# Kernel optimization log

Hardware: AMD Instinct MI355X
Metric: run time of the kernel (lower is better)

Reference implementation:

```python
import jax, jax.numpy as jnp
import numpy as np

B, S, H = 2, 2048, 2048
NH, NKV, HD = 16, 4, 128
THETA = 1000000.0

def _rope_tables(seq_len, dim, theta):
    inv_freq = 1.0 / (theta ** (np.arange(0, dim, 2, dtype=np.float32) / dim))
    t = np.arange(seq_len, dtype=np.float32)
    freqs = np.outer(t, inv_freq)                      # [S, dim/2]
    emb = np.concatenate([freqs, freqs], axis=-1)      # [S, dim]
    return jnp.asarray(np.cos(emb)), jnp.asarray(np.sin(emb))

def setup_inputs() -> dict:
    key = jax.random.key(0)
    ks = jax.random.split(key, 5)
    cos, sin = _rope_tables(S, HD, THETA)
    scale = 1.0 / np.sqrt(H)
    return {
        "x": jax.random.normal(ks[0], (B, S, H), jnp.float32),
        "cos": cos, "sin": sin,
        "wq": jax.random.normal(ks[1], (H, NH * HD), jnp.float32) * scale,
        "wk": jax.random.normal(ks[2], (H, NKV * HD), jnp.float32) * scale,
        "wv": jax.random.normal(ks[3], (H, NKV * HD), jnp.float32) * scale,
        "wo": jax.random.normal(ks[4], (NH * HD, H), jnp.float32) * scale,
    }

def _rotate_half(t):
    h = t.shape[-1] // 2
    return jnp.concatenate([-t[..., h:], t[..., :h]], axis=-1)

def reference(x, cos, sin, wq, wk, wv, wo):
    b, s, _ = x.shape
    n_rep = NH // NKV
    q = (x @ wq).reshape(b, s, NH, HD)    # [b,s,nh,hd]
    k = (x @ wk).reshape(b, s, NKV, HD)
    v = (x @ wv).reshape(b, s, NKV, HD)
    # RoPE: cos/sin [s,hd] broadcast over batch and heads
    c = cos[None, :, None, :]
    sn = sin[None, :, None, :]
    q = q * c + _rotate_half(q) * sn
    k = k * c + _rotate_half(k) * sn
    # GQA: repeat kv heads n_rep times
    k = jnp.repeat(k, n_rep, axis=2)      # [b,s,nh,hd]
    v = jnp.repeat(v, n_rep, axis=2)
    q = q.transpose(0, 2, 1, 3)           # [b,nh,s,hd]
    k = k.transpose(0, 2, 1, 3)
    v = v.transpose(0, 2, 1, 3)
    scores = jnp.einsum('bhqd,bhkd->bhqk', q, k) / jnp.sqrt(jnp.float32(HD))
    causal = jnp.tril(jnp.ones((s, s), dtype=bool))
    scores = jnp.where(causal[None, None], scores, jnp.float32(-jnp.inf))
    attn = jax.nn.softmax(scores.astype(jnp.float32), axis=-1).astype(q.dtype)
    out = jnp.einsum('bhqk,bhkd->bhqd', attn, v)
    out = out.transpose(0, 2, 1, 3).reshape(b, s, NH * HD)
    return out @ wo
```

## Files before the change

kernel.cpp:

```cpp
#include <hip/hip_runtime.h>
#include <hip/hip_bf16.h>

#define Bb 2
#define Ss 2048
#define Hh 2048
#define NH 16
#define NKV 4
#define HD 128
#define NREP (NH / NKV)
#define Mrows (Bb * Ss)
#define NQKV (NH*HD + 2*NKV*HD)

using short8 = __attribute__((ext_vector_type(8))) short;
using f32x4  = __attribute__((ext_vector_type(4))) float;

__device__ __forceinline__ unsigned short f2b(float f) {
  union { float f; unsigned u; } v; v.f = f;
  return (unsigned short)((v.u + 0x7fffu + ((v.u >> 16) & 1u)) >> 16);
}

__device__ __forceinline__ void gload16(const void* g, void* l) {
  __builtin_amdgcn_global_load_lds(
      (const __attribute__((address_space(1))) unsigned int*)g,
      (__attribute__((address_space(3))) unsigned int*)l, 16, 0, 0);
}

__global__ void prep(const float* __restrict__ x, unsigned short* __restrict__ xb,
                     const float* __restrict__ wq, const float* __restrict__ wk,
                     const float* __restrict__ wv, unsigned short* __restrict__ wqkvt,
                     const float* __restrict__ wo, unsigned short* __restrict__ wot) {
  __shared__ float tile[32][33];
  const int bid = blockIdx.x;
  const int t = threadIdx.x;
  if (bid < 8192) {
    int i = (bid * 256 + t) * 4;
    float4 f = *(const float4*)(x + i);
    ushort4 o;
    o.x = f2b(f.x); o.y = f2b(f.y); o.z = f2b(f.z); o.w = f2b(f.w);
    *(ushort4*)(xb + i) = o;
    return;
  }
  const int tx = t & 31, ty = t >> 5;
  if (bid < 8192 + 6144) {
    int idx = bid - 8192;
    int n0 = (idx % 96) * 32, k0 = (idx / 96) * 32;
    const float* src; int base, C;
    if (n0 < Hh)            { src = wq; base = 0;        C = NH * HD; }
    else if (n0 < Hh + 512) { src = wk; base = Hh;       C = NKV * HD; }
    else                    { src = wv; base = Hh + 512; C = NKV * HD; }
    int ng = n0 + tx;
    int cmg = ng;
    if (ng < Hh + 512) {
      int j = ng & 127;
      cmg = (ng & ~127) + ((j >> 5) << 4) + (j & 15) + ((j >> 4) & 1) * 64;
    }
    int col = cmg - base;
    #pragma unroll
    for (int i = ty; i < 32; i += 8)
      tile[i][tx] = src[(long)(k0 + i) * C + col];
    __syncthreads();
    #pragma unroll
    for (int i = ty; i < 32; i += 8)
      wqkvt[(long)(n0 + i) * Hh + k0 + tx] = f2b(tile[tx][i]);
  } else {
    int idx = bid - 8192 - 6144;
    int n0 = (idx % 64) * 32, k0 = (idx / 64) * 32;
    #pragma unroll
    for (int i = ty; i < 32; i += 8)
      tile[i][tx] = wo[(long)(k0 + i) * Hh + n0 + tx];
    __syncthreads();
    #pragma unroll
    for (int i = ty; i < 32; i += 8)
      wot[(long)(n0 + i) * Hh + k0 + tx] = f2b(tile[tx][i]);
  }
}

__global__ __launch_bounds__(512, 2) void gemm_qkv(const unsigned short* __restrict__ A,
                                                   const unsigned short* __restrict__ Bt,
                                                   const float* __restrict__ cosT,
                                                   const float* __restrict__ sinT,
                                                   unsigned short* __restrict__ qt,
                                                   unsigned short* __restrict__ kt,
                                                   unsigned short* __restrict__ vt) {
  __shared__ unsigned short As[2][256 * 64];
  __shared__ unsigned short Bs[2][256 * 64];
  const int t = threadIdx.x;
  const int lane = t & 63, wid = t >> 6;
  const int quad = lane >> 4, l16 = lane & 15;
  const int nt = blockIdx.x >> 4, mt = blockIdx.x & 15;
  const int n0 = nt * 256, m0 = mt * 256;
  const int wm = (wid >> 2) * 128, wn = (wid & 3) * 64;
  const bool isv = nt >= 10;
  const int Kk = Hh;

  const int sg = (lane & 7) ^ (lane >> 3);
  const int srow = wid * 8 + (lane >> 3);
  const unsigned short* Ag = A  + (long)(m0 + srow) * Kk + sg * 8;
  const unsigned short* Bg = Bt + (long)(n0 + srow) * Kk + sg * 8;

  f32x4 acc[8][4] = {};
  short8 aH[4][2], bH[2][2];

#define STAGE_A(buf, k0) { _Pragma("unroll") for (int i = 0; i < 4; i++) \
    gload16(Ag + (long)i * 64 * Kk + (k0), &As[buf][wid * 512 + i * 4096]); }
#define STAGE_B(buf, k0) { _Pragma("unroll") for (int i = 0; i < 4; i++) \
    gload16(Bg + (long)i * 64 * Kk + (k0), &Bs[buf][wid * 512 + i * 4096]); }
#define LDA(buf, mh) { _Pragma("unroll") for (int qq = 0; qq < 4; qq++) \
    _Pragma("unroll") for (int ks = 0; ks < 2; ks++) \
      aH[qq][ks] = *(const short8*)(&As[buf][(wm + (mh) * 64 + qq * 16 + l16) * 64 + \
                                             (((ks * 4 + quad) ^ (l16 & 7)) * 8)]); }
#define LDB(buf, nh) { _Pragma("unroll") for (int qq = 0; qq < 2; qq++) \
    _Pragma("unroll") for (int ks = 0; ks < 2; ks++) \
      bH[qq][ks] = *(const short8*)(&Bs[buf][(wn + (nh) * 32 + qq * 16 + l16) * 64 + \
                                             (((ks * 4 + quad) ^ (l16 & 7)) * 8)]); }
#define MM(mh, nh) { \
    if (!isv) { \
      _Pragma("unroll") for (int qq = 0; qq < 4; qq++) \
      _Pragma("unroll") for (int n2 = 0; n2 < 2; n2++) \
      _Pragma("unroll") for (int ks = 0; ks < 2; ks++) \
        acc[(mh)*4+qq][(nh)*2+n2] = __builtin_amdgcn_mfma_f32_16x16x32_bf16( \
            aH[qq][ks], bH[n2][ks], acc[(mh)*4+qq][(nh)*2+n2], 0, 0, 0); \
    } else { \
      _Pragma("unroll") for (int qq = 0; qq < 4; qq++) \
      _Pragma("unroll") for (int n2 = 0; n2 < 2; n2++) \
      _Pragma("unroll") for (int ks = 0; ks < 2; ks++) \
        acc[(mh)*4+qq][(nh)*2+n2] = __builtin_amdgcn_mfma_f32_16x16x32_bf16( \
            bH[n2][ks], aH[qq][ks], acc[(mh)*4+qq][(nh)*2+n2], 0, 0, 0); \
    } }

  STAGE_A(0, 0); STAGE_B(0, 0);
  __syncthreads();

  for (int kt2 = 0; kt2 < Kk / 64; ++kt2) {
    const int cur = kt2 & 1, nxt = cur ^ 1;
    if (kt2 + 1 < Kk / 64) {
      const long k0n = (long)(kt2 + 1) * 64;
      STAGE_A(nxt, k0n);
      STAGE_B(nxt, k0n);
    }
    LDA(cur, 0); LDB(cur, 0); MM(0, 0);
    LDB(cur, 1);              MM(0, 1);
    LDA(cur, 1);              MM(1, 1);
    LDB(cur, 0);              MM(1, 0);
    __syncthreads();
  }

#undef STAGE_A
#undef STAGE_B
#undef LDA
#undef LDB
#undef MM

  if (!isv) {
    #pragma unroll
    for (int MI = 0; MI < 8; MI++)
      #pragma unroll
      for (int r = 0; r < 4; r++) {
        int srw = m0 + wm + MI * 16 + quad * 4 + r;
        int bb = srw >> 11, s = srw & (Ss - 1);
        const float* cr = cosT + (long)s * HD;
        const float* sr = sinT + (long)s * HD;
        #pragma unroll
        for (int NI = 0; NI < 4; NI += 2) {
          int cb = n0 + wn + NI * 16;
          bool isq = cb < NH * HD;
          int hh = isq ? (cb >> 7) : ((cb - NH * HD) >> 7);
          unsigned short* dst = isq ? qt + (((long)bb * NH + hh) * Ss + s) * HD
                                    : kt + (((long)bb * NKV + hh) * Ss + s) * HD;
          int d = (((cb & 127) >> 5) << 4) + l16;
          float cc = cr[d], sn = sr[d];
          float x0 = acc[MI][NI][r], x1 = acc[MI][NI + 1][r];
          dst[d]      = f2b(x0 * cc - x1 * sn);
          dst[d + 64] = f2b(x1 * cc + x0 * sn);
        }
      }
  } else {
    #pragma unroll
    for (int MI = 0; MI < 8; MI++) {
      int srw = m0 + wm + MI * 16 + l16;
      int bb = srw >> 11, s = srw & (Ss - 1);
      #pragma unroll
      for (int NI = 0; NI < 4; NI++)
        #pragma unroll
        for (int r = 0; r < 4; r++) {
          int vcol = n0 - (NH * HD + NKV * HD) + wn + NI * 16 + quad * 4 + r;
          int kvh = vcol >> 7, d = vcol & 127;
          vt[(((long)bb * NKV + kvh) * HD + d) * Ss + s] = f2b(acc[MI][NI][r]);
        }
    }
  }
}

__global__ __launch_bounds__(256) void gemm_bt(const unsigned short* __restrict__ A,
                                               const unsigned short* __restrict__ Bt,
                                               float* __restrict__ Cv,
                                               int Mm, int Nn, int Kk) {
  __shared__ unsigned short As[128 * 64];
  __shared__ unsigned short Bs[128 * 64];
  const int t = threadIdx.x;
  const int lane = t & 63, wave = t >> 6;
  const int quad = lane >> 4, l16 = lane & 15;
  const int n0 = (blockIdx.x >> 5) * 128, m0 = (blockIdx.x & 31) * 128;
  const int wm = (wave >> 1) * 64, wn = (wave & 1) * 64;

  f32x4 acc[4][4] = {};

  const int srow = t >> 3;
  const int sgr  = (t & 7) ^ (srow & 7);
  const unsigned short* Ag = A  + (long)(m0 + srow) * Kk + sgr * 8;
  const unsigned short* Bg = Bt + (long)(n0 + srow) * Kk + sgr * 8;
  unsigned short* lA = As + (wave * 64) * 8;
  unsigned short* lB = Bs + (wave * 64) * 8;

  for (int k0 = 0; k0 < Kk; k0 += 64) {
    #pragma unroll
    for (int i = 0; i < 4; i++)
      gload16(Ag + (long)i * 32 * Kk + k0, lA + i * 256 * 8);
    #pragma unroll
    for (int i = 0; i < 4; i++)
      gload16(Bg + (long)i * 32 * Kk + k0, lB + i * 256 * 8);
    __syncthreads();

    #pragma unroll
    for (int sub = 0; sub < 2; sub++) {
      short8 af[4], bf[4];
      #pragma unroll
      for (int i = 0; i < 4; i++)
        af[i] = *(const short8*)(As + (wm + i * 16 + l16) * 64 + (((sub * 4 + quad) ^ (l16 & 7)) * 8));
      #pragma unroll
      for (int i = 0; i < 4; i++)
        bf[i] = *(const short8*)(Bs + (wn + i * 16 + l16) * 64 + (((sub * 4 + quad) ^ (l16 & 7)) * 8));

      #pragma unroll
      for (int mi = 0; mi < 4; mi++)
        #pragma unroll
        for (int ni = 0; ni < 4; ni++)
          acc[mi][ni] = __builtin_amdgcn_mfma_f32_16x16x32_bf16(af[mi], bf[ni], acc[mi][ni], 0, 0, 0);
    }
    __syncthreads();
  }

  #pragma unroll
  for (int mi = 0; mi < 4; mi++)
    #pragma unroll
    for (int ni = 0; ni < 4; ni++)
      #pragma unroll
      for (int r = 0; r < 4; r++) {
        long row = m0 + wm + mi * 16 + quad * 4 + r;
        long col = n0 + wn + ni * 16 + l16;
        Cv[row * Nn + col] = acc[mi][ni][r];
      }
}

__global__ __launch_bounds__(256, 2) void flash_attn(const unsigned short* __restrict__ qt,
                                                     const unsigned short* __restrict__ kt,
                                                     const unsigned short* __restrict__ vt,
                                                     unsigned short* __restrict__ out) {
  __shared__ unsigned short Ks[2][64 * 128];
  __shared__ unsigned short Vs[2][128 * 64];

  const int w = threadIdx.x >> 6, lane = threadIdx.x & 63;
  const int quad = lane >> 4, l16 = lane & 15;
  const int r8 = lane >> 3, c8 = lane & 7;
  const int idx = blockIdx.x;
  const int xcd = idx & 7;
  const int b = xcd >> 2, kvh = xcd & 3;
  const int rest = idx >> 3;
  const int k16 = rest >> 2;
  const int qblk = (k16 < 8) ? (15 - k16) : (k16 - 8);
  const int h = kvh * NREP + (rest & 3);
  const int q0w = qblk * 128 + w * 32;

  const unsigned short* Qb = qt + ((long)b * NH + h) * Ss * HD;
  const unsigned short* Kb = kt + ((long)b * NKV + kvh) * Ss * HD;
  const unsigned short* Vb = vt + ((long)b * NKV + kvh) * HD * Ss;
  const int nch = (qblk + 1) * 2;

  #pragma unroll
  for (int i = 0; i < 4; i++) {
    int rho = i * 16 + w * 4 + quad;
    int key = (rho & 32) + ((rho >> 2) & 3) * 8 + ((rho >> 4) & 1) * 4 + (rho & 3);
    int sg = l16 ^ (w * 4 + quad);
    gload16(Kb + (long)key * HD + sg * 8, &Ks[0][(i * 256 + w * 64) * 8]);
  }
  #pragma unroll
  for (int i = 0; i < 4; i++) {
    int dv = i * 32 + w * 8 + r8;
    int sg = c8 ^ r8;
    gload16(Vb + (long)dv * Ss + sg * 8, &Vs[0][(i * 256 + w * 64) * 8]);
  }

  short8 qf[2][4];
  #pragma unroll
  for (int qi = 0; qi < 2; qi++)
    #pragma unroll
    for (int kc = 0; kc < 4; kc++)
      qf[qi][kc] = *(const short8*)(Qb + (long)(q0w + qi * 16 + l16) * HD + kc * 32 + quad * 8);

  f32x4 accO[2][8] = {};
  float l_i[2];
  l_i[0] = l_i[1] = 0.f;
  const float cscale = 1.4426950408889634f * 0.08838834764831845f;

  for (int c = 0; c < nch; ++c) {
    const unsigned short* Ksb = Ks[c & 1];
    const unsigned short* Vsb = Vs[c & 1];

    if (c + 1 < nch) {
      const int k0 = (c + 1) * 64;
      unsigned short* Kd = Ks[(c + 1) & 1];
      unsigned short* Vd = Vs[(c + 1) & 1];
      #pragma unroll
      for (int i = 0; i < 4; i++) {
        int rho = i * 16 + w * 4 + quad;
        int key = (rho & 32) + ((rho >> 2) & 3) * 8 + ((rho >> 4) & 1) * 4 + (rho & 3);
        int sg = l16 ^ (w * 4 + quad);
        gload16(Kb + (long)(k0 + key) * HD + sg * 8, Kd + (i * 256 + w * 64) * 8);
      }
      #pragma unroll
      for (int i = 0; i < 4; i++) {
        int dv = i * 32 + w * 8 + r8;
        int sg = c8 ^ r8;
        gload16(Vb + (long)dv * Ss + k0 + sg * 8, Vd + (i * 256 + w * 64) * 8);
      }
      asm volatile("s_waitcnt vmcnt(8)" ::: "memory");
    } else {
      asm volatile("s_waitcnt vmcnt(0)" ::: "memory");
    }
    asm volatile("s_barrier" ::: "memory");

    if (c * 64 < q0w + 32) {
      f32x4 sc[2][4] = {};
      #pragma unroll
      for (int T = 0; T < 4; T++)
        #pragma unroll
        for (int kc = 0; kc < 4; kc++) {
          short8 kf = *(const short8*)(Ksb + ((16 * T + l16) * 16 + ((kc * 4 + quad) ^ l16)) * 8);
          #pragma unroll
          for (int qi = 0; qi < 2; qi++)
            sc[qi][T] = __builtin_amdgcn_mfma_f32_16x16x32_bf16(kf, qf[qi][kc], sc[qi][T], 0, 0, 0);
        }

      if ((c + 1) * 64 - 1 > q0w) {
        #pragma unroll
        for (int qi = 0; qi < 2; qi++) {
          int qq = q0w + qi * 16 + l16;
          #pragma unroll
          for (int T = 0; T < 4; T++)
            #pragma unroll
            for (int r = 0; r < 4; r++) {
              int ka = c * 64 + (T >> 1) * 32 + quad * 8 + (T & 1) * 4 + r;
              if (ka > qq) sc[qi][T][r] = -__builtin_inff();
            }
        }
      }

      short8 pf[2][2];
      #pragma unroll
      for (int qi = 0; qi < 2; qi++) {
        float p[4][4], rs = 0.f;
        #pragma unroll
        for (int T = 0; T < 4; T++)
          #pragma unroll
          for (int r = 0; r < 4; r++) {
            p[T][r] = __builtin_amdgcn_exp2f(sc[qi][T][r] * cscale);
            rs += p[T][r];
          }
        rs += __shfl_xor(rs, 16);
        rs += __shfl_xor(rs, 32);
        l_i[qi] += rs;

        #pragma unroll
        for (int c2 = 0; c2 < 2; c2++) {
          short8 f;
          f[0] = (short)f2b(p[2 * c2][0]);     f[1] = (short)f2b(p[2 * c2][1]);
          f[2] = (short)f2b(p[2 * c2][2]);     f[3] = (short)f2b(p[2 * c2][3]);
          f[4] = (short)f2b(p[2 * c2 + 1][0]); f[5] = (short)f2b(p[2 * c2 + 1][1]);
          f[6] = (short)f2b(p[2 * c2 + 1][2]); f[7] = (short)f2b(p[2 * c2 + 1][3]);
          pf[qi][c2] = f;
        }
      }

      #pragma unroll
      for (int c2 = 0; c2 < 2; c2++)
        #pragma unroll
        for (int Dt = 0; Dt < 8; Dt++) {
          short8 vf = *(const short8*)(Vsb + ((16 * Dt + l16) * 8 + ((4 * c2 + quad) ^ (l16 & 7))) * 8);
          #pragma unroll
          for (int qi = 0; qi < 2; qi++)
            accO[qi][Dt] = __builtin_amdgcn_mfma_f32_16x16x32_bf16(vf, pf[qi][c2], accO[qi][Dt], 0, 0, 0);
        }
    }

    asm volatile("s_waitcnt lgkmcnt(0)" ::: "memory");
    asm volatile("s_barrier" ::: "memory");
  }

  #pragma unroll
  for (int qi = 0; qi < 2; qi++) {
    float inv = 1.f / l_i[qi];
    long orow = (long)b * Ss + q0w + qi * 16 + l16;
    #pragma unroll
    for (int Dt = 0; Dt < 8; Dt++) {
      ushort4 o;
      o.x = f2b(accO[qi][Dt][0] * inv);
      o.y = f2b(accO[qi][Dt][1] * inv);
      o.z = f2b(accO[qi][Dt][2] * inv);
      o.w = f2b(accO[qi][Dt][3] * inv);
      *(ushort4*)(out + orow * (NH * HD) + h * HD + Dt * 16 + quad * 4) = o;
    }
  }
}

extern "C" void kernel_launch(void* const* d_in, const int* in_sizes, int n_in,
                              void* d_out, int out_size, void* d_ws, size_t ws_size,
                              hipStream_t stream) {
  const float* x    = (const float*)d_in[0];
  const float* cosT = (const float*)d_in[1];
  const float* sinT = (const float*)d_in[2];
  const float* wq   = (const float*)d_in[3];
  const float* wk   = (const float*)d_in[4];
  const float* wv   = (const float*)d_in[5];
  const float* wo   = (const float*)d_in[6];
  float* out = (float*)d_out;

  char* ws = (char*)d_ws;
  unsigned short* xb    = (unsigned short*)(ws);
  unsigned short* wqkvt = (unsigned short*)(ws + (16l << 20));
  unsigned short* wot   = (unsigned short*)(ws + (28l << 20));
  unsigned short* qt    = (unsigned short*)(ws + (36l << 20));
  unsigned short* kt    = (unsigned short*)(ws + (52l << 20));
  unsigned short* vt    = (unsigned short*)(ws + (56l << 20));
  unsigned short* attno = xb;

  prep<<<8192 + 6144 + 4096, 256, 0, stream>>>(x, xb, wq, wk, wv, wqkvt, wo, wot);

  gemm_qkv<<<(NQKV / 256) * (Mrows / 256), 512, 0, stream>>>(xb, wqkvt, cosT, sinT, qt, kt, vt);

  flash_attn<<<(Ss / 128) * NH * Bb, 256, 0, stream>>>(qt, kt, vt, attno);

  gemm_bt<<<(Hh / 128) * (Mrows / 128), 256, 0, stream>>>(attno, wot, out, Mrows, Hh, Hh);
}
```

Baseline: 324.6 us.

## Use 4-stage K=32 global-to-LDS pipeline with vmcnt waits in QKV GEMM

Replaces the double-buffered K=64 staging in the QKV projection GEMM with a four-buffer ring of K=32 tiles. Three tiles stay in flight, and explicit s_waitcnt vmcnt plus a raw s_barrier take the place of __syncthreads. The aim is to hide global-load latency behind MFMA work using the same LDS footprint. In exchange there are twice as many barriers per K, and each K step has fewer MFMAs to cover LDS reads. Correctness now depends on the vmcnt counts matching the number of outstanding loads per stage.

```diff
diff --git a/kernel.cpp b/kernel.cpp
--- a/kernel.cpp
+++ b/kernel.cpp
@@ -82,8 +82,8 @@
                                                    unsigned short* __restrict__ qt,
                                                    unsigned short* __restrict__ kt,
                                                    unsigned short* __restrict__ vt) {
-  __shared__ unsigned short As[2][256 * 64];
-  __shared__ unsigned short Bs[2][256 * 64];
+  __shared__ unsigned short As[4][256 * 32];
+  __shared__ unsigned short Bs[4][256 * 32];
   const int t = threadIdx.x;
   const int lane = t & 63, wid = t >> 6;
   const int quad = lane >> 4, l16 = lane & 15;
@@ -92,64 +92,56 @@
   const int wm = (wid >> 2) * 128, wn = (wid & 3) * 64;
   const bool isv = nt >= 10;
   const int Kk = Hh;
-
-  const int sg = (lane & 7) ^ (lane >> 3);
-  const int srow = wid * 8 + (lane >> 3);
-  const unsigned short* Ag = A  + (long)(m0 + srow) * Kk + sg * 8;
-  const unsigned short* Bg = Bt + (long)(n0 + srow) * Kk + sg * 8;
+  const int NT = Kk / 32;
+
+  const int rowA = wid * 32 + (lane >> 2);
+  const int sg2  = (lane & 3) ^ ((lane >> 2) & 3);
+  const unsigned short* Ag = A  + (long)(m0 + rowA) * Kk + sg2 * 8;
+  const unsigned short* Bg = Bt + (long)(n0 + rowA) * Kk + sg2 * 8;
 
   f32x4 acc[8][4] = {};
-  short8 aH[4][2], bH[2][2];
-
-#define STAGE_A(buf, k0) { _Pragma("unroll") for (int i = 0; i < 4; i++) \
-    gload16(Ag + (long)i * 64 * Kk + (k0), &As[buf][wid * 512 + i * 4096]); }
-#define STAGE_B(buf, k0) { _Pragma("unroll") for (int i = 0; i < 4; i++) \
-    gload16(Bg + (long)i * 64 * Kk + (k0), &Bs[buf][wid * 512 + i * 4096]); }
-#define LDA(buf, mh) { _Pragma("unroll") for (int qq = 0; qq < 4; qq++) \
-    _Pragma("unroll") for (int ks = 0; ks < 2; ks++) \
-      aH[qq][ks] = *(const short8*)(&As[buf][(wm + (mh) * 64 + qq * 16 + l16) * 64 + \
-                                             (((ks * 4 + quad) ^ (l16 & 7)) * 8)]); }
-#define LDB(buf, nh) { _Pragma("unroll") for (int qq = 0; qq < 2; qq++) \
-    _Pragma("unroll") for (int ks = 0; ks < 2; ks++) \
-      bH[qq][ks] = *(const short8*)(&Bs[buf][(wn + (nh) * 32 + qq * 16 + l16) * 64 + \
-                                             (((ks * 4 + quad) ^ (l16 & 7)) * 8)]); }
-#define MM(mh, nh) { \
+
+#define STAGE32(buf, ktile) { const long kk = (long)(ktile) * 32; \
+    _Pragma("unroll") for (int i = 0; i < 2; i++) \
+      gload16(Ag + (long)i * 16 * Kk + kk, &As[buf][(wid * 32 + i * 16) * 32]); \
+    _Pragma("unroll") for (int i = 0; i < 2; i++) \
+      gload16(Bg + (long)i * 16 * Kk + kk, &Bs[buf][(wid * 32 + i * 16) * 32]); }
+
+#define BODY(buf) { short8 af[8], bf[4]; \
+    _Pragma("unroll") for (int mi = 0; mi < 8; mi++) \
+      af[mi] = *(const short8*)(&As[buf][(wm + mi * 16 + l16) * 32 + ((quad ^ (l16 & 3)) * 8)]); \
+    _Pragma("unroll") for (int ni = 0; ni < 4; ni++) \
+      bf[ni] = *(const short8*)(&Bs[buf][(wn + ni * 16 + l16) * 32 + ((quad ^ (l16 & 3)) * 8)]); \
     if (!isv) { \
-      _Pragma("unroll") for (int qq = 0; qq < 4; qq++) \
-      _Pragma("unroll") for (int n2 = 0; n2 < 2; n2++) \
-      _Pragma("unroll") for (int ks = 0; ks < 2; ks++) \
-        acc[(mh)*4+qq][(nh)*2+n2] = __builtin_amdgcn_mfma_f32_16x16x32_bf16( \
-            aH[qq][ks], bH[n2][ks], acc[(mh)*4+qq][(nh)*2+n2], 0, 0, 0); \
+      _Pragma("unroll") for (int mi = 0; mi < 8; mi++) \
+      _Pragma("unroll") for (int ni = 0; ni < 4; ni++) \
+        acc[mi][ni] = __builtin_amdgcn_mfma_f32_16x16x32_bf16(af[mi], bf[ni], acc[mi][ni], 0, 0, 0); \
     } else { \
-      _Pragma("unroll") for (int qq = 0; qq < 4; qq++) \
-      _Pragma("unroll") for (int n2 = 0; n2 < 2; n2++) \
-      _Pragma("unroll") for (int ks = 0; ks < 2; ks++) \
-        acc[(mh)*4+qq][(nh)*2+n2] = __builtin_amdgcn_mfma_f32_16x16x32_bf16( \
-            bH[n2][ks], aH[qq][ks], acc[(mh)*4+qq][(nh)*2+n2], 0, 0, 0); \
+      _Pragma("unroll") for (int mi = 0; mi < 8; mi++) \
+      _Pragma("unroll") for (int ni = 0; ni < 4; ni++) \
+        acc[mi][ni] = __builtin_amdgcn_mfma_f32_16x16x32_bf16(bf[ni], af[mi], acc[mi][ni], 0, 0, 0); \
     } }
 
-  STAGE_A(0, 0); STAGE_B(0, 0);
-  __syncthreads();
-
-  for (int kt2 = 0; kt2 < Kk / 64; ++kt2) {
-    const int cur = kt2 & 1, nxt = cur ^ 1;
-    if (kt2 + 1 < Kk / 64) {
-      const long k0n = (long)(kt2 + 1) * 64;
-      STAGE_A(nxt, k0n);
-      STAGE_B(nxt, k0n);
-    }
-    LDA(cur, 0); LDB(cur, 0); MM(0, 0);
-    LDB(cur, 1);              MM(0, 1);
-    LDA(cur, 1);              MM(1, 1);
-    LDB(cur, 0);              MM(1, 0);
-    __syncthreads();
-  }
-
-#undef STAGE_A
-#undef STAGE_B
-#undef LDA
-#undef LDB
-#undef MM
+  STAGE32(0, 0); STAGE32(1, 1); STAGE32(2, 2);
+
+  for (int kt2 = 0; kt2 < NT - 3; ++kt2) {
+    asm volatile("s_waitcnt vmcnt(8)" ::: "memory");
+    __builtin_amdgcn_s_barrier();
+    STAGE32((kt2 + 3) & 3, kt2 + 3);
+    BODY(kt2 & 3);
+  }
+  asm volatile("s_waitcnt vmcnt(8)" ::: "memory");
+  __builtin_amdgcn_s_barrier();
+  BODY((NT - 3) & 3);
+  asm volatile("s_waitcnt vmcnt(4)" ::: "memory");
+  __builtin_amdgcn_s_barrier();
+  BODY((NT - 2) & 3);
+  asm volatile("s_waitcnt vmcnt(0)" ::: "memory");
+  __builtin_amdgcn_s_barrier();
+  BODY((NT - 1) & 3);
+
+#undef STAGE32
+#undef BODY
 
   if (!isv) {
     #pragma unroll
```

After: 657.6 us. +102.6%, slower.
